# Kernel optimization log

Hardware: AMD Instinct MI355X
Metric: run time of the kernel (lower is better)

The kernel has to match this reference:

```python
import jax, jax.numpy as jnp
import numpy as np
import itertools

B, N, G, H = 64, 1024, 256, 512
SIGMA2 = 0.01        # inlier_params[0] -> Scorer_dist sigma^2
INLIER_ALPHA = 0.5   # inlier_params[-1]


def setup_inputs() -> dict:
    key = jax.random.key(0)
    k1, k2, k3 = jax.random.split(key, 3)
    pts = jax.random.normal(k1, (B, 3, N), dtype=jnp.float32)
    target = jax.random.normal(k2, (B, 3), dtype=jnp.float32)
    pt_weight = jax.random.normal(k3, (B, N), dtype=jnp.float32)
    # idx_combi = all C(G,3) index triples; sample hyps*B rows like sample_hyp
    combos = np.fromiter(itertools.chain.from_iterable(itertools.combinations(range(G), 3)), dtype=np.int32).reshape(-1, 3)
    rng = np.random.default_rng(3627474)
    tmp = rng.integers(0, combos.shape[0], size=B * H)
    sel_idx = jnp.asarray(combos[tmp].reshape(B, H, 3), dtype=jnp.int32)
    return {"pts": pts, "target": target, "pt_weight": pt_weight, "sel_idx": sel_idx}


def reference(pts, target, pt_weight, sel_idx):
    batch = pts.shape[0]
    pts_t = jnp.transpose(pts, (0, 2, 1))                       # [B, N, 3]
    # topk point selection by learned weights (sorted flag irrelevant to the math)
    _, idx = jax.lax.top_k(pt_weight, G)                        # [B, G]
    gpts = jnp.take_along_axis(pts_t, idx[:, :, None], axis=1)  # [B, G, 3]
    # gather 3 random points per hypothesis -> plane (utils.pts_to_plane)
    tri = gpts[jnp.arange(batch)[:, None, None], sel_idx]       # [B, H, 3pts, 3dims]
    p0, p1, p2 = tri[:, :, 0], tri[:, :, 1], tri[:, :, 2]
    n = jnp.cross(p1 - p0, p2 - p0)                             # [B, H, 3]
    d = -jnp.sum(n * p0, axis=-1, keepdims=True)                # [B, H, 1]
    planes = jnp.concatenate([n, d], axis=-1)                   # [B, H, 4]
    # degenerate-plane fallback (tries==1 branch in sample_hyp)
    all_zero = jnp.all(planes == 0, axis=-1, keepdims=True)
    planes = jnp.where(all_zero, jnp.ones_like(planes), planes)
    # normalize by ||normal||
    nrm = jnp.sqrt(jnp.sum(planes[:, :, :3] ** 2, axis=-1, keepdims=True))
    planes = planes / nrm
    # Scorer_dist: |a x + b y + c z + d| over all points, gaussian score, sum
    dists = jnp.abs(jnp.einsum("bhc,bcn->bhn", planes[:, :, :3], pts) + planes[:, :, 3:4])  # [B,H,N]
    score = jnp.sum(jnp.exp(-(dists ** 2) / (2.0 * SIGMA2)), axis=2)                         # [B,H]
    # ms_euclidean loss between hypothesis normals and target normal
    normals = planes[:, :, :3]
    t = target[:, None, :]
    loss = jnp.minimum(jnp.sum((normals - t) ** 2, axis=2), jnp.sum((normals + t) ** 2, axis=2))  # [B,H]
    maxindex = jnp.argmax(score, axis=1)                        # [B]
    ar = jnp.arange(batch)
    top_loss = loss[ar, maxindex]                               # [B]
    pred = normals[ar, maxindex]                                # [B, 3]
    w = jax.nn.softmax(INLIER_ALPHA * score, axis=1)
    exp_loss = jnp.sum(loss * w, axis=1)                        # [B]
    return exp_loss, top_loss, pred, gpts
```

## Files before the change

kernel.cpp:

```cpp
#include <hip/hip_runtime.h>

#define B 64
#define N 1024
#define G 256
#define H 512

#define S_SCALE 8.4932183f
#define INV_S   (1.0f / S_SCALE)

__device__ __forceinline__ float exp2_fast(float x) {
#if __has_builtin(__builtin_amdgcn_exp2f)
    return __builtin_amdgcn_exp2f(x);
#else
    return __expf(x * 0.69314718056f);
#endif
}

#define TKB 4

__global__ __launch_bounds__(1024) void topk_gather_kernel(
    const float* __restrict__ pts,
    const float* __restrict__ pt_weight,
    float* __restrict__ out_gpts)
{
    const int b = blockIdx.x / TKB;
    const int q = blockIdx.x % TKB;
    const int tid = threadIdx.x;

    __shared__ float w[N];
    __shared__ int part[4][256];

    w[tid] = pt_weight[(size_t)b * N + tid];
    __syncthreads();

    const int e = tid & 255;
    const int p = tid >> 8;
    const int i = (q << 8) + e;
    const float wi = w[i];
    const float* wq = w + (p << 8);

    int r = 0;
    if (p < q) {
        #pragma unroll 8
        for (int j = 0; j < 256; j += 4) {
            const float4 wj = *(const float4*)(wq + j);
            r += (wj.x >= wi) + (wj.y >= wi) + (wj.z >= wi) + (wj.w >= wi);
        }
    } else if (p > q) {
        #pragma unroll 8
        for (int j = 0; j < 256; j += 4) {
            const float4 wj = *(const float4*)(wq + j);
            r += (wj.x > wi) + (wj.y > wi) + (wj.z > wi) + (wj.w > wi);
        }
    } else {
        const int j0 = p << 8;
        #pragma unroll 8
        for (int j = 0; j < 256; j += 4) {
            const float4 wj = *(const float4*)(wq + j);
            r += (wj.x > wi) || (wj.x == wi && (j0 + j + 0) < i);
            r += (wj.y > wi) || (wj.y == wi && (j0 + j + 1) < i);
            r += (wj.z > wi) || (wj.z == wi && (j0 + j + 2) < i);
            r += (wj.w > wi) || (wj.w == wi && (j0 + j + 3) < i);
        }
    }
    part[p][e] = r;
    __syncthreads();

    if (p == 0) {
        const int rank = part[0][e] + part[1][e] + part[2][e] + part[3][e];
        if (rank < G) {
            float* dst = out_gpts + ((size_t)b * G + rank) * 3;
            dst[0] = pts[b * 3 * N + 0 * N + i];
            dst[1] = pts[b * 3 * N + 1 * N + i];
            dst[2] = pts[b * 3 * N + 2 * N + i];
        }
    }
}

__global__ __launch_bounds__(256) void plane_score_kernel(
    const float* __restrict__ pts,
    const float* __restrict__ target,
    const int* __restrict__ sel_idx,
    const float* __restrict__ gpts,
    float* __restrict__ score,
    float* __restrict__ loss,
    float* __restrict__ normals)
{
    __shared__ float sp[3 * N];
    __shared__ float gp[3 * G];
    const int blk = blockIdx.x;
    const int tid = threadIdx.x;
    const int b   = blk >> 4;
    const int hg  = blk & 15;
    const int wave = tid >> 6;
    const int lane = tid & 63;

    {
        const float4* ps = (const float4*)(pts + (size_t)b * 3 * N);
        float4* spv = (float4*)sp;
        spv[tid]       = ps[tid];
        spv[tid + 256] = ps[tid + 256];
        spv[tid + 512] = ps[tid + 512];
        if (tid < 192)
            ((float4*)gp)[tid] = ((const float4*)(gpts + (size_t)b * 3 * G))[tid];
    }
    __syncthreads();

    const int h0 = (hg << 5) + (wave << 3);
    float nx[8], ny[8], nz[8], pd[8], acc[8];

    #pragma unroll
    for (int hh = 0; hh < 8; ++hh) {
        const int* si = sel_idx + ((size_t)b * H + h0 + hh) * 3;
        const int g0 = si[0] * 3, g1 = si[1] * 3, g2 = si[2] * 3;
        const float p0x = gp[g0], p0y = gp[g0 + 1], p0z = gp[g0 + 2];
        const float p1x = gp[g1], p1y = gp[g1 + 1], p1z = gp[g1 + 2];
        const float p2x = gp[g2], p2y = gp[g2 + 1], p2z = gp[g2 + 2];
        const float e1x = p1x - p0x, e1y = p1y - p0y, e1z = p1z - p0z;
        const float e2x = p2x - p0x, e2y = p2y - p0y, e2z = p2z - p0z;
        float x = e1y * e2z - e1z * e2y;
        float y = e1z * e2x - e1x * e2z;
        float z = e1x * e2y - e1y * e2x;
        float d = -(x * p0x + y * p0y + z * p0z);
        if (x == 0.f && y == 0.f && z == 0.f && d == 0.f) { x = y = z = d = 1.f; }
        const float ns = S_SCALE / sqrtf(x * x + y * y + z * z);
        nx[hh] = x * ns; ny[hh] = y * ns; nz[hh] = z * ns; pd[hh] = d * ns;
        acc[hh] = 0.f;
    }

    #pragma unroll 4
    for (int k = 0; k < N / 64; ++k) {
        const int n = lane + (k << 6);
        const float px = sp[n], py = sp[N + n], pz = sp[2 * N + n];
        #pragma unroll
        for (int hh = 0; hh < 8; ++hh) {
            const float u = fmaf(nx[hh], px, fmaf(ny[hh], py, fmaf(nz[hh], pz, pd[hh])));
            acc[hh] += exp2_fast(-(u * u));
        }
    }

    const float tx = target[b * 3 + 0], ty = target[b * 3 + 1], tz = target[b * 3 + 2];
    #pragma unroll
    for (int hh = 0; hh < 8; ++hh) {
        float a = acc[hh];
        #pragma unroll
        for (int off = 32; off; off >>= 1) a += __shfl_xor(a, off);
        if (lane == 0) {
            const float x = nx[hh] * INV_S, y = ny[hh] * INV_S, z = nz[hh] * INV_S;
            const float l1 = (x - tx) * (x - tx) + (y - ty) * (y - ty) + (z - tz) * (z - tz);
            const float l2 = (x + tx) * (x + tx) + (y + ty) * (y + ty) + (z + tz) * (z + tz);
            const int idx = b * H + h0 + hh;
            score[idx] = a;
            loss[idx] = fminf(l1, l2);
            normals[idx * 3 + 0] = x;
            normals[idx * 3 + 1] = y;
            normals[idx * 3 + 2] = z;
        }
    }
}

__global__ __launch_bounds__(256) void finalize_kernel(
    const float* __restrict__ score,
    const float* __restrict__ loss,
    const float* __restrict__ normals,
    float* __restrict__ out)
{
    const int b = blockIdx.x;
    const int tid = threadIdx.x;
    const int wave = tid >> 6;
    const int lane = tid & 63;

    __shared__ float sv[4]; __shared__ int sidx[4];
    __shared__ float ssw[4], sswl[4];
    __shared__ float s_max; __shared__ int s_maxi;

    const float* sc = score + b * H;
    const float* ls = loss + b * H;
    const float s0 = sc[tid], s1 = sc[tid + 256];

    float v; int vi;
    if (s1 > s0) { v = s1; vi = tid + 256; } else { v = s0; vi = tid; }
    #pragma unroll
    for (int off = 32; off; off >>= 1) {
        const float v2 = __shfl_xor(v, off);
        const int i2 = __shfl_xor(vi, off);
        if (v2 > v || (v2 == v && i2 < vi)) { v = v2; vi = i2; }
    }
    if (lane == 0) { sv[wave] = v; sidx[wave] = vi; }
    __syncthreads();

    if (tid == 0) {
        float bv = sv[0]; int bi = sidx[0];
        #pragma unroll
        for (int k = 1; k < 4; ++k) {
            if (sv[k] > bv || (sv[k] == bv && sidx[k] < bi)) { bv = sv[k]; bi = sidx[k]; }
        }
        s_max = bv; s_maxi = bi;
    }
    __syncthreads();

    const float m = s_max;
    const float w0 = __expf(0.5f * (s0 - m)), w1 = __expf(0.5f * (s1 - m));
    float tw = w0 + w1;
    float twl = w0 * ls[tid] + w1 * ls[tid + 256];
    #pragma unroll
    for (int off = 32; off; off >>= 1) {
        tw += __shfl_xor(tw, off);
        twl += __shfl_xor(twl, off);
    }
    if (lane == 0) { ssw[wave] = tw; sswl[wave] = twl; }
    __syncthreads();

    if (tid == 0) {
        const float TW = ssw[0] + ssw[1] + ssw[2] + ssw[3];
        const float TWL = sswl[0] + sswl[1] + sswl[2] + sswl[3];
        const int mi = s_maxi;
        out[b] = TWL / TW;
        out[B + b] = ls[mi];
        out[2 * B + b * 3 + 0] = normals[((size_t)b * H + mi) * 3 + 0];
        out[2 * B + b * 3 + 1] = normals[((size_t)b * H + mi) * 3 + 1];
        out[2 * B + b * 3 + 2] = normals[((size_t)b * H + mi) * 3 + 2];
    }
}

extern "C" void kernel_launch(void* const* d_in, const int* in_sizes, int n_in,
                              void* d_out, int out_size, void* d_ws, size_t ws_size,
                              hipStream_t stream) {
    const float* pts       = (const float*)d_in[0];
    const float* target    = (const float*)d_in[1];
    const float* pt_weight = (const float*)d_in[2];
    const int*   sel_idx   = (const int*)d_in[3];

    float* out = (float*)d_out;
    float* out_gpts = out + 5 * B;

    float* ws      = (float*)d_ws;
    float* score   = ws;
    float* loss    = ws + B * H;
    float* normals = ws + 2 * B * H;

    topk_gather_kernel<<<B * TKB, 1024, 0, stream>>>(pts, pt_weight, out_gpts);
    plane_score_kernel<<<B * 16, 256, 0, stream>>>(pts, target, sel_idx, out_gpts,
                                                   score, loss, normals);
    finalize_kernel<<<B, 256, 0, stream>>>(score, loss, normals, out);
}
```

Measured before the change: 33.55 us.

## Fuse finalize into plane scoring via last-block-per-batch atomic counter

Removes the separate finalize launch. Each plane-scoring block writes its scores, losses and normals with agent-scope stores, then bumps a per-batch atomic counter. The 16th block to arrive for a batch does the argmax and softmax reduction, reading the data back with agent-scope loads. The topk kernel resets the counter. This saves one kernel launch and its dependency gap, at the cost of an atomic and some memory-ordering care using relaxed atomics plus a waitcnt.

```diff
diff --git a/kernel.cpp b/kernel.cpp
--- a/kernel.cpp
+++ b/kernel.cpp
@@ -16,12 +16,20 @@
 #endif
 }
 
+__device__ __forceinline__ void st_agent(float* p, float v) {
+    __hip_atomic_store(p, v, __ATOMIC_RELAXED, __HIP_MEMORY_SCOPE_AGENT);
+}
+__device__ __forceinline__ float ld_agent(const float* p) {
+    return __hip_atomic_load(p, __ATOMIC_RELAXED, __HIP_MEMORY_SCOPE_AGENT);
+}
+
 #define TKB 4
 
 __global__ __launch_bounds__(1024) void topk_gather_kernel(
     const float* __restrict__ pts,
     const float* __restrict__ pt_weight,
-    float* __restrict__ out_gpts)
+    float* __restrict__ out_gpts,
+    int* __restrict__ cnt)
 {
     const int b = blockIdx.x / TKB;
     const int q = blockIdx.x % TKB;
@@ -31,6 +39,7 @@
     __shared__ int part[4][256];
 
     w[tid] = pt_weight[(size_t)b * N + tid];
+    if (q == 0 && tid == 0) cnt[b] = 0;
     __syncthreads();
 
     const int e = tid & 255;
@@ -77,17 +86,24 @@
     }
 }
 
-__global__ __launch_bounds__(256) void plane_score_kernel(
+__global__ __launch_bounds__(256) void plane_finalize_kernel(
     const float* __restrict__ pts,
     const float* __restrict__ target,
     const int* __restrict__ sel_idx,
     const float* __restrict__ gpts,
+    float* __restrict__ out,
     float* __restrict__ score,
     float* __restrict__ loss,
-    float* __restrict__ normals)
+    float* __restrict__ normals,
+    int* __restrict__ cnt)
 {
     __shared__ float sp[3 * N];
     __shared__ float gp[3 * G];
+    __shared__ float sv[4]; __shared__ int sidx[4];
+    __shared__ float ssw[4], sswl[4];
+    __shared__ float s_max; __shared__ int s_maxi;
+    __shared__ bool s_last;
+
     const int blk = blockIdx.x;
     const int tid = threadIdx.x;
     const int b   = blk >> 4;
@@ -150,76 +166,73 @@
             const float l1 = (x - tx) * (x - tx) + (y - ty) * (y - ty) + (z - tz) * (z - tz);
             const float l2 = (x + tx) * (x + tx) + (y + ty) * (y + ty) + (z + tz) * (z + tz);
             const int idx = b * H + h0 + hh;
-            score[idx] = a;
-            loss[idx] = fminf(l1, l2);
-            normals[idx * 3 + 0] = x;
-            normals[idx * 3 + 1] = y;
-            normals[idx * 3 + 2] = z;
-        }
-    }
-}
-
-__global__ __launch_bounds__(256) void finalize_kernel(
-    const float* __restrict__ score,
-    const float* __restrict__ loss,
-    const float* __restrict__ normals,
-    float* __restrict__ out)
-{
-    const int b = blockIdx.x;
-    const int tid = threadIdx.x;
-    const int wave = tid >> 6;
-    const int lane = tid & 63;
-
-    __shared__ float sv[4]; __shared__ int sidx[4];
-    __shared__ float ssw[4], sswl[4];
-    __shared__ float s_max; __shared__ int s_maxi;
-
-    const float* sc = score + b * H;
-    const float* ls = loss + b * H;
-    const float s0 = sc[tid], s1 = sc[tid + 256];
-
-    float v; int vi;
-    if (s1 > s0) { v = s1; vi = tid + 256; } else { v = s0; vi = tid; }
-    #pragma unroll
-    for (int off = 32; off; off >>= 1) {
-        const float v2 = __shfl_xor(v, off);
-        const int i2 = __shfl_xor(vi, off);
-        if (v2 > v || (v2 == v && i2 < vi)) { v = v2; vi = i2; }
-    }
-    if (lane == 0) { sv[wave] = v; sidx[wave] = vi; }
-    __syncthreads();
-
+            st_agent(&score[idx], a);
+            st_agent(&loss[idx], fminf(l1, l2));
+            st_agent(&normals[idx * 3 + 0], x);
+            st_agent(&normals[idx * 3 + 1], y);
+            st_agent(&normals[idx * 3 + 2], z);
+        }
+    }
+
+    asm volatile("s_waitcnt vmcnt(0)" ::: "memory");
+    __syncthreads();
     if (tid == 0) {
-        float bv = sv[0]; int bi = sidx[0];
-        #pragma unroll
-        for (int k = 1; k < 4; ++k) {
-            if (sv[k] > bv || (sv[k] == bv && sidx[k] < bi)) { bv = sv[k]; bi = sidx[k]; }
-        }
-        s_max = bv; s_maxi = bi;
-    }
-    __syncthreads();
-
-    const float m = s_max;
-    const float w0 = __expf(0.5f * (s0 - m)), w1 = __expf(0.5f * (s1 - m));
-    float tw = w0 + w1;
-    float twl = w0 * ls[tid] + w1 * ls[tid + 256];
-    #pragma unroll
-    for (int off = 32; off; off >>= 1) {
-        tw += __shfl_xor(tw, off);
-        twl += __shfl_xor(twl, off);
-    }
-    if (lane == 0) { ssw[wave] = tw; sswl[wave] = twl; }
-    __syncthreads();
-
-    if (tid == 0) {
-        const float TW = ssw[0] + ssw[1] + ssw[2] + ssw[3];
-        const float TWL = sswl[0] + sswl[1] + sswl[2] + sswl[3];
-        const int mi = s_maxi;
-        out[b] = TWL / TW;
-        out[B + b] = ls[mi];
-        out[2 * B + b * 3 + 0] = normals[((size_t)b * H + mi) * 3 + 0];
-        out[2 * B + b * 3 + 1] = normals[((size_t)b * H + mi) * 3 + 1];
-        out[2 * B + b * 3 + 2] = normals[((size_t)b * H + mi) * 3 + 2];
+        const int prev = __hip_atomic_fetch_add(&cnt[b], 1, __ATOMIC_RELAXED,
+                                                __HIP_MEMORY_SCOPE_AGENT);
+        s_last = (prev == 15);
+    }
+    __syncthreads();
+    if (!s_last) return;
+
+    {
+        const float* sc = score + b * H;
+        const float* ls = loss + b * H;
+        const float s0 = ld_agent(&sc[tid]),       s1 = ld_agent(&sc[tid + 256]);
+        const float l0 = ld_agent(&ls[tid]),       l1 = ld_agent(&ls[tid + 256]);
+
+        float v; int vi;
+        if (s1 > s0) { v = s1; vi = tid + 256; } else { v = s0; vi = tid; }
+        #pragma unroll
+        for (int off = 32; off; off >>= 1) {
+            const float v2 = __shfl_xor(v, off);
+            const int i2 = __shfl_xor(vi, off);
+            if (v2 > v || (v2 == v && i2 < vi)) { v = v2; vi = i2; }
+        }
+        if (lane == 0) { sv[wave] = v; sidx[wave] = vi; }
+        __syncthreads();
+
+        if (tid == 0) {
+            float bv = sv[0]; int bi = sidx[0];
+            #pragma unroll
+            for (int k = 1; k < 4; ++k) {
+                if (sv[k] > bv || (sv[k] == bv && sidx[k] < bi)) { bv = sv[k]; bi = sidx[k]; }
+            }
+            s_max = bv; s_maxi = bi;
+        }
+        __syncthreads();
+
+        const float m = s_max;
+        const float w0 = __expf(0.5f * (s0 - m)), w1 = __expf(0.5f * (s1 - m));
+        float tw = w0 + w1;
+        float twl = w0 * l0 + w1 * l1;
+        #pragma unroll
+        for (int off = 32; off; off >>= 1) {
+            tw += __shfl_xor(tw, off);
+            twl += __shfl_xor(twl, off);
+        }
+        if (lane == 0) { ssw[wave] = tw; sswl[wave] = twl; }
+        __syncthreads();
+
+        if (tid == 0) {
+            const float TW = ssw[0] + ssw[1] + ssw[2] + ssw[3];
+            const float TWL = sswl[0] + sswl[1] + sswl[2] + sswl[3];
+            const int mi = s_maxi;
+            out[b] = TWL / TW;
+            out[B + b] = ld_agent(&ls[mi]);
+            out[2 * B + b * 3 + 0] = ld_agent(&normals[((size_t)b * H + mi) * 3 + 0]);
+            out[2 * B + b * 3 + 1] = ld_agent(&normals[((size_t)b * H + mi) * 3 + 1]);
+            out[2 * B + b * 3 + 2] = ld_agent(&normals[((size_t)b * H + mi) * 3 + 2]);
+        }
     }
 }
 
@@ -238,9 +251,9 @@
     float* score   = ws;
     float* loss    = ws + B * H;
     float* normals = ws + 2 * B * H;
-
-    topk_gather_kernel<<<B * TKB, 1024, 0, stream>>>(pts, pt_weight, out_gpts);
-    plane_score_kernel<<<B * 16, 256, 0, stream>>>(pts, target, sel_idx, out_gpts,
-                                                   score, loss, normals);
-    finalize_kernel<<<B, 256, 0, stream>>>(score, loss, normals, out);
-}
+    int*   cnt     = (int*)(ws + 5 * B * H);
+
+    topk_gather_kernel<<<B * TKB, 1024, 0, stream>>>(pts, pt_weight, out_gpts, cnt);
+    plane_finalize_kernel<<<B * 16, 256, 0, stream>>>(pts, target, sel_idx, out_gpts,
+                                                      out, score, loss, normals, cnt);
+}
```

Result: slower. 35.15 us (+4.8%).
